# Kernel tuning notes

Measured on AMD Instinct MI355X. Metric: run time of the kernel, lower is better.

The kernel has to match this reference:

```python
import jax, jax.numpy as jnp
import numpy as np

Q_BITS = 8
GELU_A = -0.2888
GELU_B = -1.769
INV_SQRT2 = 0.7071067811865476


def _ste_round(x):
    # straight-through round (identity grad)
    return x + jax.lax.stop_gradient(jnp.round(x) - x)


def fake_quant_weight(w):
    # per-tensor symmetric int8 fake quant
    qmax = 2.0 ** (Q_BITS - 1) - 1.0  # 127
    s = jnp.maximum(jnp.max(jnp.abs(w)), 1e-8) / qmax
    q = jnp.clip(_ste_round(w / s), -qmax - 1.0, qmax)
    return q * s


def fake_quant_act(x):
    # per-tensor asymmetric uint8 fake quant
    levels = 2.0 ** Q_BITS - 1.0  # 255
    xmin = jax.lax.stop_gradient(jnp.min(x))
    xmax = jax.lax.stop_gradient(jnp.max(x))
    s = jnp.maximum(xmax - xmin, 1e-8) / levels
    zp = jnp.round(-xmin / s)
    q = jnp.clip(_ste_round(x / s) + zp, 0.0, levels)
    return (q - zp) * s


def int_gelu(x):
    # I-BERT polynomial GELU: gelu(x) = x * 0.5 * (1 + L(x/sqrt(2)))
    # L(t) = sign(t) * (a * (clip(|t|, 0, -b) + b)^2 + 1)
    t = x * INV_SQRT2
    at = jnp.minimum(jnp.abs(t), -GELU_B)
    L = jnp.sign(t) * (GELU_A * (at + GELU_B) ** 2 + 1.0)
    return x * 0.5 * (1.0 + L)


def setup_inputs() -> dict:
    key = jax.random.key(0)
    k = jax.random.split(key, 5)
    B, S, D, H = 64, 197, 768, 3072
    x = jax.random.normal(k[0], (B, S, D), dtype=jnp.float32)
    w1 = jax.random.normal(k[1], (H, D), dtype=jnp.float32) * (1.0 / np.sqrt(D))
    b1 = jax.random.normal(k[2], (H,), dtype=jnp.float32) * 0.02
    w2 = jax.random.normal(k[3], (D, H), dtype=jnp.float32) * (1.0 / np.sqrt(H))
    b2 = jax.random.normal(k[4], (D,), dtype=jnp.float32) * 0.02
    return {"x": x, "w1": w1, "b1": b1, "w2": w2, "b2": b2}


def reference(x, w1, b1, w2, b2):
    # QuantLinear 1: fake-quant act + weight, then GEMM
    xq = fake_quant_act(x)
    h = jnp.einsum('bsd,hd->bsh', xq, fake_quant_weight(w1)) + b1
    # IntGELU (dropout is identity in eval)
    g = int_gelu(h)
    # QuantLinear 2
    gq = fake_quant_act(g)
    out = jnp.einsum('bsh,dh->bsd', gq, fake_quant_weight(w2)) + b2
    return out
```

## Files before the change

### kernel.cpp

```cpp
#include <hip/hip_runtime.h>
#include <stdint.h>
#include <stddef.h>

typedef int v4i  __attribute__((ext_vector_type(4)));
typedef int v16i __attribute__((ext_vector_type(16)));
typedef _Float16 vh8 __attribute__((ext_vector_type(8)));

#define GELU_A   (-0.2888f)
#define GELU_B   (-1.769f)
#define INV_SQRT2 0.70710678118654752440f

#define GLD16(gp, lp) __builtin_amdgcn_global_load_lds( \
    (const __attribute__((address_space(1))) unsigned int*)(gp), \
    (__attribute__((address_space(3))) unsigned int*)(lp), 16, 0, 0)

#define WAIT_VM4 0x0F74
#define WAIT_VM0 0x0F70


__device__ __forceinline__ unsigned enc_f(float f){
  unsigned u = __float_as_uint(f);
  return (u & 0x80000000u) ? ~u : (u | 0x80000000u);
}
__device__ __forceinline__ float dec_f(unsigned e){
  unsigned u = (e & 0x80000000u) ? (e & 0x7FFFFFFFu) : ~e;
  return __uint_as_float(u);
}

__device__ __forceinline__ float int_gelu_f(float x){
  float t = x * INV_SQRT2;
  float at = fminf(fabsf(t), 1.769f);
  float u = at + GELU_B;
  float p = GELU_A * (u * u) + 1.0f;
  float L = (t > 0.0f) ? p : ((t < 0.0f) ? -p : 0.0f);
  return x * 0.5f * (1.0f + L);
}

__global__ __launch_bounds__(256) void reduce_stats(
    const float4* __restrict__ x, int nx4,
    const float4* __restrict__ w1, int n14,
    const float4* __restrict__ w2, int n24,
    unsigned* __restrict__ sc)
{
  __shared__ float ra[256], rb[256];
  const int tid = threadIdx.x;
  const int b = blockIdx.x;
  if (b < 1024){
    float lmin = 3.4e38f, lmax = -3.4e38f;
    for (long i = (long)b * 256 + tid; i < nx4; i += 1024L * 256L){
      float4 v = x[i];
      lmin = fminf(lmin, fminf(fminf(v.x, v.y), fminf(v.z, v.w)));
      lmax = fmaxf(lmax, fmaxf(fmaxf(v.x, v.y), fmaxf(v.z, v.w)));
    }
    ra[tid] = lmin; rb[tid] = lmax;
    __syncthreads();
    for (int s = 128; s > 0; s >>= 1){
      if (tid < s){ ra[tid] = fminf(ra[tid], ra[tid + s]); rb[tid] = fmaxf(rb[tid], rb[tid + s]); }
      __syncthreads();
    }
    if (tid == 0){
      atomicMin(&sc[0], enc_f(ra[0]));
      atomicMax(&sc[2], enc_f(rb[0]));
    }
  } else {
    const float4* w; int n4; int slot; int bl;
    if (b < 1152){ w = w1; n4 = n14; slot = 3; bl = b - 1024; }
    else         { w = w2; n4 = n24; slot = 4; bl = b - 1152; }
    float la = 0.0f;
    for (long i = (long)bl * 256 + tid; i < n4; i += 128L * 256L){
      float4 v = w[i];
      la = fmaxf(la, fmaxf(fmaxf(fabsf(v.x), fabsf(v.y)), fmaxf(fabsf(v.z), fabsf(v.w))));
    }
    ra[tid] = la;
    __syncthreads();
    for (int s = 128; s > 0; s >>= 1){
      if (tid < s) ra[tid] = fmaxf(ra[tid], ra[tid + s]);
      __syncthreads();
    }
    if (tid == 0) atomicMax(&sc[slot], __float_as_uint(ra[0]));
  }
}

__global__ __launch_bounds__(256) void quant_all(
    const float4* __restrict__ x, unsigned* __restrict__ qx, long nx4,
    const float* __restrict__ w1, const float* __restrict__ w2,
    int8_t* __restrict__ qw1, int8_t* __restrict__ qw2,
    int* __restrict__ rs1, int* __restrict__ rs2,
    const unsigned* __restrict__ sc, int H, int D)
{
  const int tid = threadIdx.x;
  const int b = blockIdx.x;
  if (b < 2048){
    const float vmin = dec_f(sc[0]);
    const float vmax = dec_f(sc[2]);
    const float s  = fmaxf(vmax - vmin, 1e-8f) / 255.0f;
    const float zp = rintf(-vmin / s);
    for (long i = (long)b * 256 + tid; i < nx4; i += 2048L * 256L){
      float4 v = x[i];
      int q0 = (int)fminf(fmaxf(rintf(v.x / s) + zp, 0.0f), 255.0f) - 128;
      int q1 = (int)fminf(fmaxf(rintf(v.y / s) + zp, 0.0f), 255.0f) - 128;
      int q2 = (int)fminf(fmaxf(rintf(v.z / s) + zp, 0.0f), 255.0f) - 128;
      int q3 = (int)fminf(fmaxf(rintf(v.w / s) + zp, 0.0f), 255.0f) - 128;
      qx[i] = ((unsigned)(q0 & 255)) | ((unsigned)(q1 & 255) << 8) |
              ((unsigned)(q2 & 255) << 16) | ((unsigned)(q3 & 255) << 24);
    }
  } else {
    __shared__ int red[256];
    const int wb = b - 2048;
    const float* w; int8_t* q; int* rs; int K; int n; float s;
    if (wb < H){ w = w1; q = qw1; rs = rs1; K = D; n = wb;
                 s = fmaxf(__uint_as_float(sc[3]), 1e-8f) / 127.0f; }
    else       { w = w2; q = qw2; rs = rs2; K = H; n = wb - H;
                 s = fmaxf(__uint_as_float(sc[4]), 1e-8f) / 127.0f; }
    int sum = 0;
    for (int k = tid; k < K; k += 256){
      float v = w[(size_t)n * K + k];
      float qf = fminf(fmaxf(rintf(v / s), -128.0f), 127.0f);
      int qi = (int)qf;
      q[(size_t)n * K + k] = (int8_t)qi;
      sum += qi;
    }
    red[tid] = sum;
    __syncthreads();
    for (int st = 128; st > 0; st >>= 1){
      if (tid < st) red[tid] += red[tid + st];
      __syncthreads();
    }
    if (tid == 0) rs[n] = red[0];
  }
}

__global__ __launch_bounds__(256) void quant_g(
    const vh8* __restrict__ g, uint2* __restrict__ qg, long n8,
    const unsigned* __restrict__ sc)
{
  const float gmin = dec_f(sc[1]), gmax = dec_f(sc[5]);
  const float qs  = fmaxf(gmax - gmin, 1e-8f) / 255.0f;
  const float qzp = rintf(-gmin / qs);
  const long stride = (long)gridDim.x * blockDim.x;
  for (long i = (long)blockIdx.x * blockDim.x + threadIdx.x; i < n8; i += stride){
    vh8 v = g[i];
    unsigned lo = 0, hi = 0;
#pragma unroll
    for (int j = 0; j < 4; j++){
      int q = (int)fminf(fmaxf(rintf((float)v[j] / qs) + qzp, 0.0f), 255.0f) - 128;
      lo |= ((unsigned)(q & 255)) << (8 * j);
    }
#pragma unroll
    for (int j = 0; j < 4; j++){
      int q = (int)fminf(fmaxf(rintf((float)v[4 + j] / qs) + qzp, 0.0f), 255.0f) - 128;
      hi |= ((unsigned)(q & 255)) << (8 * j);
    }
    uint2 o; o.x = lo; o.y = hi;
    qg[i] = o;
  }
}

template<int MODE>
__global__ __launch_bounds__(256) void gemm_i8(
    const int8_t* __restrict__ A, const int8_t* __restrict__ Bm,
    const int* __restrict__ rowsum, const float* __restrict__ bias,
    void* __restrict__ Cout, int M, int N, int K,
    unsigned* __restrict__ sc)
{
  __shared__ __align__(16) int8_t lds[3][16384];

  const int tid  = threadIdx.x;
  const int lane = tid & 63;
  const int wave = tid >> 6;
  const int l31  = lane & 31;
  const int kh   = lane >> 5;
  const int n0   = blockIdx.x * 128;
  const int m0   = blockIdx.y * 128;
  const int wm   = (wave & 1) * 64;
  const int wn   = (wave >> 1) * 64;

  int aoffs[2], boffs[2];
  const int ldst[2] = { wave * 2048, wave * 2048 + 1024 };
#pragma unroll
  for (int t = 0; t < 2; t++){
    int rowl = wave * 32 + t * 16 + (lane >> 2);
    int csw  = ((lane & 3) ^ ((rowl >> 1) & 3)) << 4;
    int ga = m0 + rowl; if (ga >= M) ga = M - 1;
    aoffs[t] = ga * K + csw;
    boffs[t] = (n0 + rowl) * K + csw;
  }

  const int w2  = (l31 >> 1) & 3;
  const int sA0 = (kh ^ w2) << 4;
  int arow[2], brow[2];
#pragma unroll
  for (int mi = 0; mi < 2; mi++){
    arow[mi] = (wm + mi * 32 + l31) * 64;
    brow[mi] = (wn + mi * 32 + l31) * 64;
  }

  v16i acc[2][2] = {};
  const int NT = K >> 6;

#pragma unroll
  for (int t = 0; t < 2; t++){
    GLD16(A  + aoffs[t],      &lds[0][ldst[t]]);
    GLD16(Bm + boffs[t],      &lds[0][8192 + ldst[t]]);
  }
#pragma unroll
  for (int t = 0; t < 2; t++){
    GLD16(A  + aoffs[t] + 64, &lds[1][ldst[t]]);
    GLD16(Bm + boffs[t] + 64, &lds[1][8192 + ldst[t]]);
  }

  for (int kt = 0; kt < NT; kt++){
    const int8_t* buf = lds[kt % 3];
    if (kt + 1 < NT) __builtin_amdgcn_s_waitcnt(WAIT_VM4);
    else             __builtin_amdgcn_s_waitcnt(WAIT_VM0);
    __builtin_amdgcn_s_barrier();
    __builtin_amdgcn_sched_barrier(0);

    v4i af[2][2], bf[2][2];
#pragma unroll
    for (int kk = 0; kk < 2; kk++){
      const int sb = sA0 ^ (kk << 5);
#pragma unroll
      for (int mi = 0; mi < 2; mi++){
        af[kk][mi] = *(const v4i*)(buf + arow[mi] + sb);
        bf[kk][mi] = *(const v4i*)(buf + 8192 + brow[mi] + sb);
      }
    }

    if (kt + 2 < NT){
      int8_t* nbuf = lds[(kt + 2) % 3];
      const int ko = (kt + 2) << 6;
#pragma unroll
      for (int t = 0; t < 2; t++){
        GLD16(A  + aoffs[t] + ko, nbuf + ldst[t]);
        GLD16(Bm + boffs[t] + ko, nbuf + 8192 + ldst[t]);
      }
    }

#pragma unroll
    for (int kk = 0; kk < 2; kk++)
#pragma unroll
      for (int mi = 0; mi < 2; mi++)
#pragma unroll
        for (int nj = 0; nj < 2; nj++)
          acc[mi][nj] = __builtin_amdgcn_mfma_i32_32x32x32_i8(af[kk][mi], bf[kk][nj], acc[mi][nj], 0, 0, 0);
  }

  float s_h, off_h;
  if constexpr (MODE == 1){
    float gmin = dec_f(sc[1]), gmax = dec_f(sc[5]);
    float sg = fmaxf(gmax - gmin, 1e-8f) / 255.0f;
    float zp = rintf(-gmin / sg);
    float sw = fmaxf(__uint_as_float(sc[4]), 1e-8f) / 127.0f;
    s_h = sg * sw; off_h = 128.0f - zp;
  } else {
    float xmin = dec_f(sc[0]), xmax = dec_f(sc[2]);
    float sx = fmaxf(xmax - xmin, 1e-8f) / 255.0f;
    float zp = rintf(-xmin / sx);
    float sw = fmaxf(__uint_as_float(sc[3]), 1e-8f) / 127.0f;
    s_h = sx * sw; off_h = 128.0f - zp;
  }
  float qs = 1.0f, qzp = 0.0f;
  if constexpr (MODE == 2){
    float gmin = dec_f(sc[1]), gmax = dec_f(sc[5]);
    qs = fmaxf(gmax - gmin, 1e-8f) / 255.0f;
    qzp = rintf(-gmin / qs);
  }

  float lmin = 3.4e38f, lmax = -3.4e38f;
#pragma unroll
  for (int nj = 0; nj < 2; nj++){
    const int n = n0 + wn + nj * 32 + l31;
    const float rsv = off_h * (float)rowsum[n];
    const float bv = bias[n];
#pragma unroll
    for (int mi = 0; mi < 2; mi++){
      const int mbase = m0 + wm + mi * 32 + 4 * kh;
#pragma unroll
      for (int r = 0; r < 16; r++){
        const int m = mbase + (r & 3) + 8 * (r >> 2);
        if (m < M){
          float h = s_h * ((float)acc[mi][nj][r] + rsv) + bv;
          if constexpr (MODE == 0){
            float gv = int_gelu_f(h);
            lmin = fminf(lmin, gv); lmax = fmaxf(lmax, gv);
          } else if constexpr (MODE == 3){
            float gv = int_gelu_f(h);
            lmin = fminf(lmin, gv); lmax = fmaxf(lmax, gv);
            ((_Float16*)Cout)[(size_t)m * N + n] = (_Float16)gv;
          } else if constexpr (MODE == 2){
            float gv = int_gelu_f(h);
            float qf = fminf(fmaxf(rintf(gv / qs) + qzp, 0.0f), 255.0f);
            ((int8_t*)Cout)[(size_t)m * N + n] = (int8_t)((int)qf - 128);
          } else {
            ((float*)Cout)[(size_t)m * N + n] = h;
          }
        }
      }
    }
  }

  if constexpr (MODE == 0 || MODE == 3){
    __syncthreads();
    float* redA = (float*)&lds[0][0];
    float* redB = ((float*)&lds[0][0]) + 256;
    redA[tid] = lmin; redB[tid] = lmax;
    __syncthreads();
    for (int st = 128; st > 0; st >>= 1){
      if (tid < st){
        redA[tid] = fminf(redA[tid], redA[tid + st]);
        redB[tid] = fmaxf(redB[tid], redB[tid + st]);
      }
      __syncthreads();
    }
    if (tid == 0){
      atomicMin(&sc[1], enc_f(redA[0]));
      atomicMax(&sc[5], enc_f(redB[0]));
    }
  }
}

extern "C" void kernel_launch(void* const* d_in, const int* in_sizes, int n_in,
                              void* d_out, int out_size, void* d_ws, size_t ws_size,
                              hipStream_t stream)
{
  const float* x  = (const float*)d_in[0];
  const float* w1 = (const float*)d_in[1];
  const float* b1 = (const float*)d_in[2];
  const float* w2 = (const float*)d_in[3];
  const float* b2 = (const float*)d_in[4];
  float* out = (float*)d_out;

  const int H = in_sizes[2];
  const int D = in_sizes[4];
  const int M = in_sizes[0] / D;

  char* ws = (char*)d_ws;
  unsigned* sc = (unsigned*)ws;
  size_t off = 256;
  int8_t* qx  = (int8_t*)(ws + off); off += (size_t)M * D;
  int8_t* qw1 = (int8_t*)(ws + off); off += (size_t)H * D;
  int8_t* qw2 = (int8_t*)(ws + off); off += (size_t)D * H;
  int* rs1 = (int*)(ws + off); off += (size_t)H * 4;
  int* rs2 = (int*)(ws + off); off += 4096;
  int8_t* qg  = (int8_t*)(ws + off); off += (size_t)M * H;
  _Float16* g16 = (_Float16*)(ws + off);
  const size_t need_big = off + (size_t)M * H * 2;
  (void)n_in; (void)out_size;

  hipMemsetAsync(sc, 0xFF, 8, stream);
  hipMemsetAsync(sc + 2, 0x00, 16, stream);

  reduce_stats<<<dim3(1280), dim3(256), 0, stream>>>(
      (const float4*)x, M * D / 4,
      (const float4*)w1, H * D / 4,
      (const float4*)w2, D * H / 4, sc);

  quant_all<<<dim3(2048 + H + D), dim3(256), 0, stream>>>(
      (const float4*)x, (unsigned*)qx, (long)M * D / 4,
      w1, w2, qw1, qw2, rs1, rs2, sc, H, D);

  const dim3 g1(H / 128, (M + 127) / 128), g2(D / 128, (M + 127) / 128), blk(256);

  if (ws_size >= need_big){
    gemm_i8<3><<<g1, blk, 0, stream>>>(qx, qw1, rs1, b1, g16, M, H, D, sc);
    quant_g<<<dim3(2048), blk, 0, stream>>>(
        (const vh8*)g16, (uint2*)qg, (long)M * H / 8, sc);
  } else {
    gemm_i8<0><<<g1, blk, 0, stream>>>(qx, qw1, rs1, b1, nullptr, M, H, D, sc);
    gemm_i8<2><<<g1, blk, 0, stream>>>(qx, qw1, rs1, b1, qg, M, H, D, sc);
  }

  gemm_i8<1><<<g2, blk, 0, stream>>>(qg, qw2, rs2, b2, out, M, D, H, sc);
}
```

Baseline: 309.3 us.

## Pre-swizzle int8 weights into MFMA fragment layout and load B directly to registers

The weight quantization kernel now writes int8 weights in a blocked layout matching the 32x32x32 MFMA B-fragment, using vectorized float4 reads and 16-byte stores. The GEMM loads B fragments straight from global memory into double-buffered registers instead of staging them through LDS. This halves LDS per block and allows an occupancy hint of 3 blocks per CU. The cost is more vector registers and exposed global-load latency for B. The new weight loop only covers K up to 16*256, which holds for D=768 and H=3072.

```diff
diff --git a/kernel.cpp b/kernel.cpp
--- a/kernel.cpp
+++ b/kernel.cpp
@@ -14,8 +14,8 @@
     (const __attribute__((address_space(1))) unsigned int*)(gp), \
     (__attribute__((address_space(3))) unsigned int*)(lp), 16, 0, 0)
 
-#define WAIT_VM4 0x0F74
-#define WAIT_VM0 0x0F70
+#define WAIT_VM2   0x0F72
+#define WAIT_VM0   0x0F70
 
 
 __device__ __forceinline__ unsigned enc_f(float f){
@@ -113,12 +113,25 @@
     else       { w = w2; q = qw2; rs = rs2; K = H; n = wb - H;
                  s = fmaxf(__uint_as_float(sc[4]), 1e-8f) / 127.0f; }
     int sum = 0;
-    for (int k = tid; k < K; k += 256){
-      float v = w[(size_t)n * K + k];
-      float qf = fminf(fmaxf(rintf(v / s), -128.0f), 127.0f);
-      int qi = (int)qf;
-      q[(size_t)n * K + k] = (int8_t)qi;
-      sum += qi;
+    const int c = tid;
+    if (c < (K >> 4)){
+      const float4* wp = (const float4*)(w + (size_t)n * K + (size_t)c * 16);
+      uint4 o; unsigned wds[4];
+#pragma unroll
+      for (int q4 = 0; q4 < 4; q4++){
+        float4 v = wp[q4];
+        int qa = (int)fminf(fmaxf(rintf(v.x / s), -128.0f), 127.0f);
+        int qb = (int)fminf(fmaxf(rintf(v.y / s), -128.0f), 127.0f);
+        int qc = (int)fminf(fmaxf(rintf(v.z / s), -128.0f), 127.0f);
+        int qd = (int)fminf(fmaxf(rintf(v.w / s), -128.0f), 127.0f);
+        sum += qa + qb + qc + qd;
+        wds[q4] = ((unsigned)(qa & 255)) | ((unsigned)(qb & 255) << 8) |
+                  ((unsigned)(qc & 255) << 16) | ((unsigned)(qd & 255) << 24);
+      }
+      o.x = wds[0]; o.y = wds[1]; o.z = wds[2]; o.w = wds[3];
+      size_t off = ((((size_t)(n >> 5)) * (K >> 5) + (c >> 1)) << 10)
+                 + ((size_t)(c & 1) << 9) + ((n & 31) << 4);
+      *(uint4*)(q + off) = o;
     }
     red[tid] = sum;
     __syncthreads();
@@ -157,13 +170,13 @@
 }
 
 template<int MODE>
-__global__ __launch_bounds__(256) void gemm_i8(
-    const int8_t* __restrict__ A, const int8_t* __restrict__ Bm,
+__global__ __launch_bounds__(256, 3) void gemm_h(
+    const int8_t* __restrict__ A, const int8_t* __restrict__ Bf,
     const int* __restrict__ rowsum, const float* __restrict__ bias,
     void* __restrict__ Cout, int M, int N, int K,
     unsigned* __restrict__ sc)
 {
-  __shared__ __align__(16) int8_t lds[3][16384];
+  __shared__ __align__(16) int8_t lds[3][8192];
 
   const int tid  = threadIdx.x;
   const int lane = tid & 63;
@@ -174,77 +187,82 @@
   const int m0   = blockIdx.y * 128;
   const int wm   = (wave & 1) * 64;
   const int wn   = (wave >> 1) * 64;
-
-  int aoffs[2], boffs[2];
-  const int ldst[2] = { wave * 2048, wave * 2048 + 1024 };
+  const int NT   = K >> 6;
+  const int NKB  = K >> 5;
+
+  int aoffs[2];
+  const int ldstA[2] = { wave * 2048, wave * 2048 + 1024 };
 #pragma unroll
   for (int t = 0; t < 2; t++){
     int rowl = wave * 32 + t * 16 + (lane >> 2);
     int csw  = ((lane & 3) ^ ((rowl >> 1) & 3)) << 4;
     int ga = m0 + rowl; if (ga >= M) ga = M - 1;
     aoffs[t] = ga * K + csw;
-    boffs[t] = (n0 + rowl) * K + csw;
   }
 
   const int w2  = (l31 >> 1) & 3;
   const int sA0 = (kh ^ w2) << 4;
-  int arow[2], brow[2];
-#pragma unroll
-  for (int mi = 0; mi < 2; mi++){
-    arow[mi] = (wm + mi * 32 + l31) * 64;
-    brow[mi] = (wn + mi * 32 + l31) * 64;
+  int arow[2];
+#pragma unroll
+  for (int mi = 0; mi < 2; mi++) arow[mi] = (wm + mi * 32 + l31) * 64;
+
+  const int8_t* bpt[2];
+#pragma unroll
+  for (int nj = 0; nj < 2; nj++){
+    int cb = (n0 + wn + nj * 32) >> 5;
+    bpt[nj] = Bf + ((size_t)cb * NKB) * 1024 + lane * 16;
   }
 
   v16i acc[2][2] = {};
-  const int NT = K >> 6;
-
-#pragma unroll
-  for (int t = 0; t < 2; t++){
-    GLD16(A  + aoffs[t],      &lds[0][ldst[t]]);
-    GLD16(Bm + boffs[t],      &lds[0][8192 + ldst[t]]);
-  }
-#pragma unroll
-  for (int t = 0; t < 2; t++){
-    GLD16(A  + aoffs[t] + 64, &lds[1][ldst[t]]);
-    GLD16(Bm + boffs[t] + 64, &lds[1][8192 + ldst[t]]);
-  }
-
-  for (int kt = 0; kt < NT; kt++){
-    const int8_t* buf = lds[kt % 3];
-    if (kt + 1 < NT) __builtin_amdgcn_s_waitcnt(WAIT_VM4);
-    else             __builtin_amdgcn_s_waitcnt(WAIT_VM0);
-    __builtin_amdgcn_s_barrier();
-    __builtin_amdgcn_sched_barrier(0);
-
-    v4i af[2][2], bf[2][2];
-#pragma unroll
-    for (int kk = 0; kk < 2; kk++){
-      const int sb = sA0 ^ (kk << 5);
-#pragma unroll
-      for (int mi = 0; mi < 2; mi++){
-        af[kk][mi] = *(const v4i*)(buf + arow[mi] + sb);
-        bf[kk][mi] = *(const v4i*)(buf + 8192 + brow[mi] + sb);
-      }
-    }
-
-    if (kt + 2 < NT){
-      int8_t* nbuf = lds[(kt + 2) % 3];
-      const int ko = (kt + 2) << 6;
-#pragma unroll
-      for (int t = 0; t < 2; t++){
-        GLD16(A  + aoffs[t] + ko, nbuf + ldst[t]);
-        GLD16(Bm + boffs[t] + ko, nbuf + 8192 + ldst[t]);
-      }
-    }
-
-#pragma unroll
-    for (int kk = 0; kk < 2; kk++)
-#pragma unroll
-      for (int mi = 0; mi < 2; mi++)
-#pragma unroll
-        for (int nj = 0; nj < 2; nj++)
-          acc[mi][nj] = __builtin_amdgcn_mfma_i32_32x32x32_i8(af[kk][mi], bf[kk][nj], acc[mi][nj], 0, 0, 0);
-  }
+  v4i b0[2][2], b1[2][2];
+
+#pragma unroll
+  for (int t = 0; t < 2; t++) GLD16(A + aoffs[t], &lds[0][ldstA[t]]);
+#pragma unroll
+  for (int kk = 0; kk < 2; kk++)
+#pragma unroll
+    for (int nj = 0; nj < 2; nj++)
+      b0[kk][nj] = *(const v4i*)(bpt[nj] + (kk << 10));
+#pragma unroll
+  for (int t = 0; t < 2; t++) GLD16(A + aoffs[t] + 64, &lds[1][ldstA[t]]);
+
+  int bcur = 0, bst = 2;
+
+#define ITER(KT, BC, BN_) do{                                                  \
+    if ((KT) + 1 < NT) __builtin_amdgcn_s_waitcnt(WAIT_VM2);                   \
+    else               __builtin_amdgcn_s_waitcnt(WAIT_VM0);                   \
+    __builtin_amdgcn_s_barrier();                                              \
+    __builtin_amdgcn_sched_barrier(0);                                         \
+    const int8_t* buf = &lds[bcur][0];                                         \
+    v4i af[2][2];                                                              \
+    _Pragma("unroll") for (int kk = 0; kk < 2; kk++)                           \
+      _Pragma("unroll") for (int mi = 0; mi < 2; mi++)                         \
+        af[kk][mi] = *(const v4i*)(buf + arow[mi] + (sA0 ^ (kk << 5)));        \
+    if ((KT) + 1 < NT){                                                        \
+      const int fb = 2 * ((KT) + 1);                                           \
+      _Pragma("unroll") for (int kk = 0; kk < 2; kk++)                         \
+        _Pragma("unroll") for (int nj = 0; nj < 2; nj++)                       \
+          BN_[kk][nj] = *(const v4i*)(bpt[nj] + ((fb + kk) << 10));            \
+    }                                                                          \
+    if ((KT) + 2 < NT){                                                        \
+      const int ko = ((KT) + 2) << 6;                                          \
+      _Pragma("unroll") for (int t = 0; t < 2; t++)                            \
+        GLD16(A + aoffs[t] + ko, &lds[bst][ldstA[t]]);                         \
+    }                                                                          \
+    __builtin_amdgcn_sched_barrier(0);                                         \
+    _Pragma("unroll") for (int kk = 0; kk < 2; kk++)                           \
+      _Pragma("unroll") for (int mi = 0; mi < 2; mi++)                         \
+        _Pragma("unroll") for (int nj = 0; nj < 2; nj++)                       \
+          acc[mi][nj] = __builtin_amdgcn_mfma_i32_32x32x32_i8(af[kk][mi], BC[kk][nj], acc[mi][nj], 0, 0, 0); \
+    bcur = (bcur == 2) ? 0 : bcur + 1;                                         \
+    bst  = (bst  == 2) ? 0 : bst  + 1;                                         \
+  }while(0)
+
+  for (int kt = 0; kt < NT; kt += 2){
+    ITER(kt,     b0, b1);
+    ITER(kt + 1, b1, b0);
+  }
+#undef ITER
 
   float s_h, off_h;
   if constexpr (MODE == 1){
@@ -363,13 +381,13 @@
   const dim3 g1(H / 128, (M + 127) / 128), g2(D / 128, (M + 127) / 128), blk(256);
 
   if (ws_size >= need_big){
-    gemm_i8<3><<<g1, blk, 0, stream>>>(qx, qw1, rs1, b1, g16, M, H, D, sc);
-    quant_g<<<dim3(2048), blk, 0, stream>>>(
+    gemm_h<3><<<g1, blk, 0, stream>>>(qx, qw1, rs1, b1, g16, M, H, D, sc);
+    quant_g<<<dim3(2048), dim3(256), 0, stream>>>(
         (const vh8*)g16, (uint2*)qg, (long)M * H / 8, sc);
   } else {
-    gemm_i8<0><<<g1, blk, 0, stream>>>(qx, qw1, rs1, b1, nullptr, M, H, D, sc);
-    gemm_i8<2><<<g1, blk, 0, stream>>>(qx, qw1, rs1, b1, qg, M, H, D, sc);
-  }
-
-  gemm_i8<1><<<g2, blk, 0, stream>>>(qg, qw2, rs2, b2, out, M, D, H, sc);
-}
+    gemm_h<0><<<g1, blk, 0, stream>>>(qx, qw1, rs1, b1, nullptr, M, H, D, sc);
+    gemm_h<2><<<g1, blk, 0, stream>>>(qx, qw1, rs1, b1, qg, M, H, D, sc);
+  }
+
+  gemm_h<1><<<g2, blk, 0, stream>>>(qg, qw2, rs2, b2, out, M, D, H, sc);
+}
```

After: 332.4 us. 7.5% more time.
